# Optimization experiments

Hardware: AMD Instinct MI355X
Metric: run time of the kernel (lower is better)

Reference implementation:

```python
import jax, jax.numpy as jnp
import numpy as np
import math

B, T, C, H = 2, 2048, 1024, 16

def setup_inputs() -> dict:
    key = jax.random.key(0)
    ks = jax.random.split(key, 5)
    s = 0.02
    return {
        "x": jax.random.normal(ks[0], (B, T, C), dtype=jnp.float32),
        "W_attn": jax.random.normal(ks[1], (C, 3 * C), dtype=jnp.float32) * s,
        "b_attn": jnp.zeros((3 * C,), dtype=jnp.float32),
        "W_proj": jax.random.normal(ks[2], (C, C), dtype=jnp.float32) * s,
        "b_proj": jnp.zeros((C,), dtype=jnp.float32),
    }

def reference(x, W_attn, b_attn, W_proj, b_proj):
    Bx, Tx, Cx = x.shape
    hd = Cx // H  # head dim = 64
    qkv = x @ W_attn + b_attn                      # [B,T,3C]
    q, k, v = jnp.split(qkv, 3, axis=-1)
    # [B,H,T,hd]
    q = q.reshape(Bx, Tx, H, hd).transpose(0, 2, 1, 3)
    k = k.reshape(Bx, Tx, H, hd).transpose(0, 2, 1, 3)
    v = v.reshape(Bx, Tx, H, hd).transpose(0, 2, 1, 3)
    scale = 1.0 / math.sqrt(hd)
    att = jnp.einsum('bhqd,bhkd->bhqk', q, k) * scale   # [B,H,T,T]
    causal = jnp.tril(jnp.ones((Tx, Tx), dtype=bool))
    att = jnp.where(causal[None, None, :, :], att, -jnp.inf)
    att = jax.nn.softmax(att, axis=-1)
    y = jnp.einsum('bhqk,bhkd->bhqd', att, v)           # [B,H,T,hd]
    y = y.transpose(0, 2, 1, 3).reshape(Bx, Tx, Cx)
    return y @ W_proj + b_proj
```

## Files before the change

### kernel.cpp

```cpp
#include <hip/hip_runtime.h>

typedef __attribute__((ext_vector_type(8))) __bf16 bf16x8;
typedef __attribute__((ext_vector_type(4))) float f32x4;

#define T_SEQ 2048
#define NH 16
#define HD 64
#define CDIM 1024
#define NQK 2048
#define NQKV 3072
#define MTOT 4096

#define SWZ(r, c) ((((r) * 8) + ((c) ^ ((r) & 7))) * 8)

__device__ __forceinline__ void async_load16(const void* g, void* l) {
    __builtin_amdgcn_global_load_lds(
        (const __attribute__((address_space(1))) void*)g,
        (__attribute__((address_space(3))) void*)l, 16, 0, 0);
}

__global__ __launch_bounds__(256) void cvt_bf16_kernel(const float* __restrict__ in,
                                                       __bf16* __restrict__ out, int n) {
    int i = (blockIdx.x * 256 + threadIdx.x) * 8;
    if (i + 8 <= n) {
        float4 f0 = *(const float4*)(in + i);
        float4 f1 = *(const float4*)(in + i + 4);
        bf16x8 o;
        o[0] = (__bf16)f0.x; o[1] = (__bf16)f0.y; o[2] = (__bf16)f0.z; o[3] = (__bf16)f0.w;
        o[4] = (__bf16)f1.x; o[5] = (__bf16)f1.y; o[6] = (__bf16)f1.z; o[7] = (__bf16)f1.w;
        *(bf16x8*)(out + i) = o;
    }
}

__global__ __launch_bounds__(256) void transpose2_kernel(
    const float* __restrict__ Wa, const float* __restrict__ Wp,
    __bf16* __restrict__ WaT, __bf16* __restrict__ WpT) {
    __shared__ float tile[32][33];
    const float* in; __bf16* out; int C, bx = blockIdx.x;
    if (bx < 96) { in = Wa; out = WaT; C = 3072; }
    else         { in = Wp; out = WpT; C = 1024; bx -= 96; }
    int c0 = bx * 32, r0 = blockIdx.y * 32;
    int tx = threadIdx.x, ty = threadIdx.y;
#pragma unroll
    for (int i = 0; i < 4; i++)
        tile[ty + i * 8][tx] = in[(size_t)(r0 + ty + i * 8) * C + c0 + tx];
    __syncthreads();
#pragma unroll
    for (int i = 0; i < 4; i++)
        out[(size_t)(c0 + ty + i * 8) * 1024 + r0 + tx] = (__bf16)tile[tx][ty + i * 8];
}

template <int WNW>
__global__ __launch_bounds__(256) void gemm_bt_kernel(
    const __bf16* __restrict__ A, const __bf16* __restrict__ Bt,
    const float* __restrict__ bias, int M, int N, int K, int mode,
    __bf16* __restrict__ qkb, __bf16* __restrict__ vtb, float* __restrict__ outf)
{
    constexpr int MI = (WNW == 2) ? 4 : 2;
    constexpr int BROWS = WNW * 64;
    __shared__ __bf16 As[128 * 64];
    __shared__ __bf16 Bs[BROWS * 64];

    int tid = threadIdx.x;
    int lane = tid & 63, wid = tid >> 6;
    int quad = lane >> 4, r16 = lane & 15;
    int wm = (WNW == 2) ? (wid >> 1) * 64 : wid * 32;
    int wn = (WNW == 2) ? (wid & 1) * 64 : 0;
    int bm = blockIdx.y * 128, bn = blockIdx.x * (WNW * 64);

    f32x4 acc[MI][4] = {};

    int lrow = lane >> 3;
    int lcolsw = (((lane & 7) ^ (lrow & 7)) * 8);
    const __bf16* Ag = A + (size_t)(bm + wid * 32 + lrow) * K + lcolsw;
    const __bf16* Bg = Bt + (size_t)(bn + wid * (BROWS / 4) + lrow) * K + lcolsw;
    char* lA = (char*)As + wid * 4096;
    char* lB = (char*)Bs + wid * (BROWS / 4) * 128;

    for (int kt = 0; kt < K; kt += 64) {
        __syncthreads();
#pragma unroll
        for (int i = 0; i < 4; i++)
            async_load16(Ag + kt + (size_t)i * 8 * K, lA + i * 1024);
#pragma unroll
        for (int i = 0; i < BROWS / 32; i++)
            async_load16(Bg + kt + (size_t)i * 8 * K, lB + i * 1024);
        __syncthreads();
#pragma unroll
        for (int ks = 0; ks < 2; ks++) {
            bf16x8 af[MI], bfr[4];
#pragma unroll
            for (int i = 0; i < MI; i++)
                af[i] = *(const bf16x8*)&As[SWZ(wm + i * 16 + r16, ks * 4 + quad)];
#pragma unroll
            for (int i = 0; i < 4; i++)
                bfr[i] = *(const bf16x8*)&Bs[SWZ(wn + i * 16 + r16, ks * 4 + quad)];
#pragma unroll
            for (int mi = 0; mi < MI; mi++)
#pragma unroll
                for (int ni = 0; ni < 4; ni++)
                    acc[mi][ni] = __builtin_amdgcn_mfma_f32_16x16x32_bf16(
                        af[mi], bfr[ni], acc[mi][ni], 0, 0, 0);
        }
    }

    const float SC2 = 0.125f * 1.44269504088896f;
#pragma unroll
    for (int mi = 0; mi < MI; mi++) {
#pragma unroll
        for (int ni = 0; ni < 4; ni++) {
            int col = bn + wn + ni * 16 + r16;
            float bv = bias[col];
            int row0 = bm + wm + mi * 16 + quad * 4;
            if (mode == 1) {
#pragma unroll
                for (int rg = 0; rg < 4; rg++)
                    outf[(size_t)(row0 + rg) * N + col] = acc[mi][ni][rg] + bv;
            } else if (col < 1024) {
#pragma unroll
                for (int rg = 0; rg < 4; rg++)
                    qkb[(size_t)(row0 + rg) * NQK + col] = (__bf16)((acc[mi][ni][rg] + bv) * SC2);
            } else if (col < 2048) {
#pragma unroll
                for (int rg = 0; rg < 4; rg++)
                    qkb[(size_t)(row0 + rg) * NQK + col] = (__bf16)(acc[mi][ni][rg] + bv);
            } else {
                int dcol = col - 2048;
                int b = row0 >> 11, t0 = row0 & 2047;
                union { __bf16 h[4]; uint2 u; } pk;
#pragma unroll
                for (int rg = 0; rg < 4; rg++) pk.h[rg] = (__bf16)(acc[mi][ni][rg] + bv);
                *(uint2*)&vtb[((size_t)b * 1024 + dcol) * T_SEQ + t0] = pk.u;
            }
        }
    }
}

__global__ __launch_bounds__(256) void attn_kernel(
    const __bf16* __restrict__ qkb, const __bf16* __restrict__ vtb,
    __bf16* __restrict__ y1)
{
    __shared__ __bf16 Ks[2][64 * 64];
    __shared__ __bf16 Vs[2][64 * 64];
    __shared__ __bf16 Ps[4][16][72];

    int tid = threadIdx.x;
    int lane = tid & 63, w = tid >> 6;
    int quad = lane >> 4, r16 = lane & 15;
    int bh = blockIdx.y;
    int b = bh >> 4, h = bh & 15;
    int qtA = blockIdx.x, qtB = 31 - qtA;
    int qbA = qtA * 64, qbB = qtB * 64;

    const __bf16* Qh = qkb + (size_t)b * T_SEQ * NQK + h * HD;
    const __bf16* Kh = Qh + CDIM;
    const __bf16* Vh = vtb + ((size_t)b * 1024 + h * HD) * T_SEQ;

    const float NEG_INF = -__builtin_inff();
    int lrow = lane >> 3;
    int lcolsw = (((lane & 7) ^ (lrow & 7)) * 8);

    bf16x8 qfA[2], qfB[2];
#pragma unroll
    for (int ks = 0; ks < 2; ks++) {
        qfA[ks] = *(const bf16x8*)(Qh + (size_t)(qbA + w * 16 + r16) * NQK + ks * 32 + quad * 8);
        qfB[ks] = *(const bf16x8*)(Qh + (size_t)(qbB + w * 16 + r16) * NQK + ks * 32 + quad * 8);
    }
    f32x4 oA[4] = {}, oB[4] = {};
    float lA_ = 0.f, lB_ = 0.f;
    int g0A = qbA + w * 16, g0B = qbB + w * 16;
    int qrowA = g0A + r16, qrowB = g0B + r16;

    auto stage = [&](int kt, int buf) {
        int kb = kt * 64;
        char* lK = (char*)Ks[buf] + w * 2048;
        char* lV = (char*)Vs[buf] + w * 2048;
        const __bf16* kg = Kh + (size_t)(kb + w * 16 + lrow) * NQK + lcolsw;
        const __bf16* vg = Vh + (size_t)(w * 16 + lrow) * T_SEQ + kb + lcolsw;
        async_load16(kg, lK);
        async_load16(kg + (size_t)8 * NQK, lK + 1024);
        async_load16(vg, lV);
        async_load16(vg + (size_t)8 * T_SEQ, lV + 1024);
    };

    auto tile_compute = [&](int kb, int buf, const bf16x8 (&qf)[2], f32x4 (&o)[4],
                            float& l_i, int g0, int qrow) {
        f32x4 s[4] = {};
#pragma unroll
        for (int ks = 0; ks < 2; ks++) {
            bf16x8 kf[4];
#pragma unroll
            for (int ni = 0; ni < 4; ni++)
                kf[ni] = *(const bf16x8*)&Ks[buf][SWZ(ni * 16 + r16, ks * 4 + quad)];
#pragma unroll
            for (int ni = 0; ni < 4; ni++)
                s[ni] = __builtin_amdgcn_mfma_f32_16x16x32_bf16(kf[ni], qf[ks], s[ni], 0, 0, 0);
        }
        if (kb + 63 > g0) {
#pragma unroll
            for (int ni = 0; ni < 4; ni++)
#pragma unroll
                for (int rg = 0; rg < 4; rg++)
                    if (kb + ni * 16 + quad * 4 + rg > qrow) s[ni][rg] = NEG_INF;
        }
#pragma unroll
        for (int ni = 0; ni < 4; ni++)
#pragma unroll
            for (int rg = 0; rg < 4; rg++) {
                float p = exp2f(s[ni][rg]);
                s[ni][rg] = p;
                l_i += p;
            }
#pragma unroll
        for (int ni = 0; ni < 4; ni++) {
            union { __bf16 h[4]; uint2 u; } pk;
#pragma unroll
            for (int rg = 0; rg < 4; rg++) pk.h[rg] = (__bf16)s[ni][rg];
            *(uint2*)&Ps[w][r16][ni * 16 + quad * 4] = pk.u;
        }
#pragma unroll
        for (int ks = 0; ks < 2; ks++) {
            bf16x8 vf[4];
#pragma unroll
            for (int nd = 0; nd < 4; nd++)
                vf[nd] = *(const bf16x8*)&Vs[buf][SWZ(nd * 16 + r16, ks * 4 + quad)];
            bf16x8 pb = *(const bf16x8*)&Ps[w][r16][ks * 32 + quad * 8];
#pragma unroll
            for (int nd = 0; nd < 4; nd++)
                o[nd] = __builtin_amdgcn_mfma_f32_16x16x32_bf16(vf[nd], pb, o[nd], 0, 0, 0);
        }
    };

    int nktA = qtA + 1, nktB = qtB + 1;
    stage(0, 0);
    int cur = 0;
    for (int kt = 0; kt < nktB; kt++) {
        __syncthreads();
        if (kt + 1 < nktB) stage(kt + 1, cur ^ 1);
        int kb = kt * 64;
        tile_compute(kb, cur, qfB, oB, lB_, g0B, qrowB);
        if (kt < nktA)
            tile_compute(kb, cur, qfA, oA, lA_, g0A, qrowA);
        cur ^= 1;
    }

#pragma unroll
    for (int which = 0; which < 2; which++) {
        f32x4* o = which ? oB : oA;
        float rs = which ? lB_ : lA_;
        rs += __shfl_xor(rs, 16, 64);
        rs += __shfl_xor(rs, 32, 64);
        float inv = 1.f / rs;
        int t = (which ? qbB : qbA) + w * 16 + r16;
#pragma unroll
        for (int nd = 0; nd < 4; nd++) {
            union { __bf16 h[4]; uint2 u; } pk;
#pragma unroll
            for (int rg = 0; rg < 4; rg++) pk.h[rg] = (__bf16)(o[nd][rg] * inv);
            *(uint2*)&y1[(size_t)(b * T_SEQ + t) * CDIM + h * HD + nd * 16 + quad * 4] = pk.u;
        }
    }
}

extern "C" void kernel_launch(void* const* d_in, const int* in_sizes, int n_in,
                              void* d_out, int out_size, void* d_ws, size_t ws_size,
                              hipStream_t stream) {
    const float* x = (const float*)d_in[0];
    const float* W_attn = (const float*)d_in[1];
    const float* b_attn = (const float*)d_in[2];
    const float* W_proj = (const float*)d_in[3];
    const float* b_proj = (const float*)d_in[4];
    float* out = (float*)d_out;

    char* p = (char*)d_ws;
    __bf16* xb = (__bf16*)p;   p += (size_t)MTOT * CDIM * 2;
    __bf16* WaT = (__bf16*)p;  p += (size_t)3 * CDIM * CDIM * 2;
    __bf16* WpT = (__bf16*)p;  p += (size_t)CDIM * CDIM * 2;
    __bf16* qkb = (__bf16*)p;  p += (size_t)MTOT * NQK * 2;
    __bf16* vtb = (__bf16*)p;  p += (size_t)2 * 1024 * T_SEQ * 2;
    __bf16* y1 = xb;

    cvt_bf16_kernel<<<2048, 256, 0, stream>>>(x, xb, MTOT * CDIM);
    transpose2_kernel<<<dim3(128, 32), dim3(32, 8), 0, stream>>>(W_attn, W_proj, WaT, WpT);
    gemm_bt_kernel<2><<<dim3(24, 32), 256, 0, stream>>>(xb, WaT, b_attn, MTOT, NQKV, CDIM, 0,
                                                        qkb, vtb, nullptr);
    attn_kernel<<<dim3(16, 32), 256, 0, stream>>>(qkb, vtb, y1);
    gemm_bt_kernel<1><<<dim3(16, 32), 256, 0, stream>>>(y1, WpT, b_proj, MTOT, CDIM, CDIM, 1,
                                                        nullptr, nullptr, out);
}
```

Before: 188.2 us.

## Interleave A/B tile MFMAs, share K/V fragments, and compute row sums via MFMA

The attention loop now computes QK^T for both the A and B query tiles at once, reusing the same K and V fragments loaded from LDS, with P stored in separate per-tile LDS slots. The softmax row sum moves from scalar adds plus cross-lane shuffles to an extra MFMA against a ones vector over the bf16 P. The code also switches to the raw exp2 builtin and raises wave priority with s_setprio around MFMA groups. It reduces LDS reads and VALU work, but raises register pressure and makes the normalizer sum bf16-rounded probabilities.

```diff
diff --git a/kernel.cpp b/kernel.cpp
--- a/kernel.cpp
+++ b/kernel.cpp
@@ -142,7 +142,7 @@
 {
     __shared__ __bf16 Ks[2][64 * 64];
     __shared__ __bf16 Vs[2][64 * 64];
-    __shared__ __bf16 Ps[4][16][72];
+    __shared__ __bf16 Ps[2][4][16][72];
 
     int tid = threadIdx.x;
     int lane = tid & 63, w = tid >> 6;
@@ -166,8 +166,13 @@
         qfA[ks] = *(const bf16x8*)(Qh + (size_t)(qbA + w * 16 + r16) * NQK + ks * 32 + quad * 8);
         qfB[ks] = *(const bf16x8*)(Qh + (size_t)(qbB + w * 16 + r16) * NQK + ks * 32 + quad * 8);
     }
+
+    bf16x8 onesv;
+#pragma unroll
+    for (int i = 0; i < 8; i++) onesv[i] = (__bf16)1.0f;
+
     f32x4 oA[4] = {}, oB[4] = {};
-    float lA_ = 0.f, lB_ = 0.f;
+    f32x4 lA4 = {}, lB4 = {};
     int g0A = qbA + w * 16, g0B = qbB + w * 16;
     int qrowA = g0A + r16, qrowB = g0B + r16;
 
@@ -183,20 +188,8 @@
         async_load16(vg + (size_t)8 * T_SEQ, lV + 1024);
     };
 
-    auto tile_compute = [&](int kb, int buf, const bf16x8 (&qf)[2], f32x4 (&o)[4],
-                            float& l_i, int g0, int qrow) {
-        f32x4 s[4] = {};
-#pragma unroll
-        for (int ks = 0; ks < 2; ks++) {
-            bf16x8 kf[4];
-#pragma unroll
-            for (int ni = 0; ni < 4; ni++)
-                kf[ni] = *(const bf16x8*)&Ks[buf][SWZ(ni * 16 + r16, ks * 4 + quad)];
-#pragma unroll
-            for (int ni = 0; ni < 4; ni++)
-                s[ni] = __builtin_amdgcn_mfma_f32_16x16x32_bf16(kf[ni], qf[ks], s[ni], 0, 0, 0);
-        }
-        if (kb + 63 > g0) {
+    auto softmax_store = [&](f32x4 (&s)[4], int qrow, int kb, bool diag, int slot) {
+        if (diag) {
 #pragma unroll
             for (int ni = 0; ni < 4; ni++)
 #pragma unroll
@@ -204,30 +197,12 @@
                     if (kb + ni * 16 + quad * 4 + rg > qrow) s[ni][rg] = NEG_INF;
         }
 #pragma unroll
-        for (int ni = 0; ni < 4; ni++)
-#pragma unroll
-            for (int rg = 0; rg < 4; rg++) {
-                float p = exp2f(s[ni][rg]);
-                s[ni][rg] = p;
-                l_i += p;
-            }
-#pragma unroll
         for (int ni = 0; ni < 4; ni++) {
             union { __bf16 h[4]; uint2 u; } pk;
 #pragma unroll
-            for (int rg = 0; rg < 4; rg++) pk.h[rg] = (__bf16)s[ni][rg];
-            *(uint2*)&Ps[w][r16][ni * 16 + quad * 4] = pk.u;
-        }
-#pragma unroll
-        for (int ks = 0; ks < 2; ks++) {
-            bf16x8 vf[4];
-#pragma unroll
-            for (int nd = 0; nd < 4; nd++)
-                vf[nd] = *(const bf16x8*)&Vs[buf][SWZ(nd * 16 + r16, ks * 4 + quad)];
-            bf16x8 pb = *(const bf16x8*)&Ps[w][r16][ks * 32 + quad * 8];
-#pragma unroll
-            for (int nd = 0; nd < 4; nd++)
-                o[nd] = __builtin_amdgcn_mfma_f32_16x16x32_bf16(vf[nd], pb, o[nd], 0, 0, 0);
+            for (int rg = 0; rg < 4; rg++)
+                pk.h[rg] = (__bf16)__builtin_amdgcn_exp2f(s[ni][rg]);
+            *(uint2*)&Ps[slot][w][r16][ni * 16 + quad * 4] = pk.u;
         }
     };
 
@@ -237,20 +212,61 @@
     for (int kt = 0; kt < nktB; kt++) {
         __syncthreads();
         if (kt + 1 < nktB) stage(kt + 1, cur ^ 1);
-        int kb = kt * 64;
-        tile_compute(kb, cur, qfB, oB, lB_, g0B, qrowB);
-        if (kt < nktA)
-            tile_compute(kb, cur, qfA, oA, lA_, g0A, qrowA);
+        const bool doA = (kt < nktA);
+        const int kb = kt * 64;
+
+        f32x4 sB[4] = {}, sA[4] = {};
+#pragma unroll
+        for (int ks = 0; ks < 2; ks++) {
+            bf16x8 kf[4];
+#pragma unroll
+            for (int ni = 0; ni < 4; ni++)
+                kf[ni] = *(const bf16x8*)&Ks[cur][SWZ(ni * 16 + r16, ks * 4 + quad)];
+            __builtin_amdgcn_s_setprio(1);
+#pragma unroll
+            for (int ni = 0; ni < 4; ni++)
+                sB[ni] = __builtin_amdgcn_mfma_f32_16x16x32_bf16(kf[ni], qfB[ks], sB[ni], 0, 0, 0);
+            if (doA) {
+#pragma unroll
+                for (int ni = 0; ni < 4; ni++)
+                    sA[ni] = __builtin_amdgcn_mfma_f32_16x16x32_bf16(kf[ni], qfA[ks], sA[ni], 0, 0, 0);
+            }
+            __builtin_amdgcn_s_setprio(0);
+        }
+
+        softmax_store(sB, qrowB, kb, kb + 63 > g0B, 1);
+        if (doA) softmax_store(sA, qrowA, kb, kb + 63 > g0A, 0);
+
+#pragma unroll
+        for (int ks = 0; ks < 2; ks++) {
+            bf16x8 vf[4];
+#pragma unroll
+            for (int nd = 0; nd < 4; nd++)
+                vf[nd] = *(const bf16x8*)&Vs[cur][SWZ(nd * 16 + r16, ks * 4 + quad)];
+            bf16x8 pbB = *(const bf16x8*)&Ps[1][w][r16][ks * 32 + quad * 8];
+            __builtin_amdgcn_s_setprio(1);
+#pragma unroll
+            for (int nd = 0; nd < 4; nd++)
+                oB[nd] = __builtin_amdgcn_mfma_f32_16x16x32_bf16(vf[nd], pbB, oB[nd], 0, 0, 0);
+            lB4 = __builtin_amdgcn_mfma_f32_16x16x32_bf16(onesv, pbB, lB4, 0, 0, 0);
+            __builtin_amdgcn_s_setprio(0);
+            if (doA) {
+                bf16x8 pbA = *(const bf16x8*)&Ps[0][w][r16][ks * 32 + quad * 8];
+                __builtin_amdgcn_s_setprio(1);
+#pragma unroll
+                for (int nd = 0; nd < 4; nd++)
+                    oA[nd] = __builtin_amdgcn_mfma_f32_16x16x32_bf16(vf[nd], pbA, oA[nd], 0, 0, 0);
+                lA4 = __builtin_amdgcn_mfma_f32_16x16x32_bf16(onesv, pbA, lA4, 0, 0, 0);
+                __builtin_amdgcn_s_setprio(0);
+            }
+        }
         cur ^= 1;
     }
 
 #pragma unroll
     for (int which = 0; which < 2; which++) {
         f32x4* o = which ? oB : oA;
-        float rs = which ? lB_ : lA_;
-        rs += __shfl_xor(rs, 16, 64);
-        rs += __shfl_xor(rs, 32, 64);
-        float inv = 1.f / rs;
+        float inv = 1.f / (which ? lB4[0] : lA4[0]);
         int t = (which ? qbB : qbA) + w * 16 + r16;
 #pragma unroll
         for (int nd = 0; nd < 4; nd++) {
```

New measurement: 185.7 us. Within noise of the previous version (-1.3%).
